# Kernel tuning notes

Measured on AMD Instinct MI355X. Metric: run time of the kernel, lower is better.

Reference implementation:

```python
import jax, jax.numpy as jnp
import numpy as np

D = 256
BN_EPS = 1e-5
EPS = 0.0  # GINEEConv eps buffer, train_eps=False


def setup_inputs() -> dict:
    key = jax.random.key(0)
    ks = jax.random.split(key, 16)
    N, E, G = 60000, 200000, 1500
    node_features = jax.random.normal(ks[0], (N, 92), dtype=jnp.float32)
    edge_index = jax.random.randint(ks[1], (2, E), 0, N)
    atom_weights = jax.random.normal(ks[2], (E, 1), dtype=jnp.float32)
    batch = jnp.sort(jax.random.randint(ks[3], (N,), 0, G))
    s = 0.05
    return {
        "node_features": node_features,
        "edge_index": edge_index,
        "atom_weights": atom_weights,
        "batch": batch,
        "aW": jax.random.normal(ks[4], (92, D), dtype=jnp.float32) * s,
        "ab": jnp.zeros((D,), jnp.float32),
        "eW": jax.random.normal(ks[5], (1, D), dtype=jnp.float32) * s,
        "eb": jnp.zeros((D,), jnp.float32),
        "mlpW": jax.random.normal(ks[6], (3 * D, D), dtype=jnp.float32) * s,
        "mlpb": jnp.zeros((D,), jnp.float32),
        "nnW": jax.random.normal(ks[7], (D, D), dtype=jnp.float32) * s,
        "nnb": jnp.zeros((D,), jnp.float32),
        "bn_g": jax.random.normal(ks[8], (D,), dtype=jnp.float32) * 0.1 + 1.0,
        "bn_b": jax.random.normal(ks[9], (D,), dtype=jnp.float32) * 0.1,
        "bn_m": jax.random.normal(ks[10], (D,), dtype=jnp.float32) * 0.1,
        "bn_v": jax.random.uniform(ks[11], (D,), dtype=jnp.float32) + 0.5,
        "outW": jax.random.normal(ks[12], (D, 6), dtype=jnp.float32) * s,
        "outb": jnp.zeros((6,), jnp.float32),
    }


def _gine_layer(x, e_attr, row, col, mlpW, mlpb, nnW, nnb, bn_g, bn_b, bn_m, bn_v):
    # mlp(cat[x[row], x[col], e_attr]) without materializing the [E,3D] concat
    W1, W2, W3 = mlpW[:D], mlpW[D:2 * D], mlpW[2 * D:]
    new_e = x[row] @ W1 + x[col] @ W2 + e_attr @ W3 + mlpb  # [E, D]
    # message: relu(x_j + edge_attr), x_j = source nodes = edge_index[0]
    msg = jax.nn.relu(x[row] + new_e)  # [E, D]
    agg = jax.ops.segment_sum(msg, col, num_segments=x.shape[0])  # scatter-add to targets
    out = agg + (1.0 + EPS) * x  # residual
    h = out @ nnW + nnb
    h = (h - bn_m) * jax.lax.rsqrt(bn_v + BN_EPS) * bn_g + bn_b  # BN (eval stats)
    return jax.nn.relu(h), new_e


def reference(node_features, edge_index, atom_weights, batch,
              aW, ab, eW, eb, mlpW, mlpb, nnW, nnb,
              bn_g, bn_b, bn_m, bn_v, outW, outb):
    row, col = edge_index[0], edge_index[1]
    x = node_features @ aW + ab            # [N, 256]
    e_attr = atom_weights @ eW + eb        # [E, 256]
    for _ in range(4):  # 4 layers SHARING the same params (ModuleList of same module)
        x, e_attr = _gine_layer(x, e_attr, row, col, mlpW, mlpb, nnW, nnb,
                                bn_g, bn_b, bn_m, bn_v)
    pooled = jax.ops.segment_sum(x, batch, num_segments=1500)  # global_add_pool
    return pooled @ outW + outb  # [G, 6]
```

## Files before the change

### kernel.cpp

```cpp
#include <hip/hip_runtime.h>
#include <stdint.h>

#define DD 256
#define NNODE 60000
#define MPAD 60032
#define NEDGE 200000
#define NGRAPH 1500
#define NCHUNK 59

typedef __bf16 bf16x8 __attribute__((ext_vector_type(8)));
typedef float f32x4 __attribute__((ext_vector_type(4)));
typedef unsigned short us8 __attribute__((ext_vector_type(8)));

__device__ __forceinline__ unsigned short f2bf(float f) {
    union { float f; unsigned int u; } v; v.f = f;
    unsigned int r = v.u + 0x7FFFu + ((v.u >> 16) & 1u);
    return (unsigned short)(r >> 16);
}
__device__ __forceinline__ float bf2f(unsigned short h) {
    union { unsigned int u; float f; } v; v.u = ((unsigned int)h) << 16;
    return v.f;
}
__device__ __forceinline__ void gload_lds16(const void* g, void* l) {
    __builtin_amdgcn_global_load_lds((const __attribute__((address_space(1))) void*)g,
                                     (__attribute__((address_space(3))) void*)l, 16, 0, 0);
}

__global__ __launch_bounds__(256) void prep_weights(const float* __restrict__ mlpW,
                                                    const float* __restrict__ nnW,
                                                    const float* __restrict__ aW,
                                                    const float* __restrict__ ab,
                                                    unsigned short* __restrict__ wc1,
                                                    unsigned short* __restrict__ wc2,
                                                    unsigned short* __restrict__ nnt,
                                                    unsigned short* __restrict__ aWt) {
    int idx = blockIdx.x * 256 + threadIdx.x;
    if (idx < 256 * 512) {
        int n = idx >> 9, k = idx & 511;
        float v1 = (k < 256) ? mlpW[k * DD + n] : mlpW[(k + 256) * DD + n];
        wc1[idx] = f2bf(v1);
        wc2[idx] = f2bf(mlpW[(k + 256) * DD + n]);
    }
    if (idx < 256 * 256) {
        int n = idx >> 8, k = idx & 255;
        nnt[idx] = f2bf(nnW[k * DD + n]);
    }
    if (idx < 256 * 96) {
        int n = idx / 96, k = idx - n * 96;
        float v = (k < 92) ? aW[k * DD + n] : (k == 92 ? ab[n] : 0.0f);
        aWt[idx] = f2bf(v);
    }
}

__global__ __launch_bounds__(256) void prep_uv(const float* __restrict__ eW, const float* __restrict__ eb,
                                               const float* __restrict__ mlpW, const float* __restrict__ mlpb,
                                               const float* __restrict__ nnb,
                                               const float* __restrict__ bn_g, const float* __restrict__ bn_b,
                                               const float* __restrict__ bn_m, const float* __restrict__ bn_v,
                                               float* __restrict__ u_all, float* __restrict__ v_all,
                                               float* __restrict__ scale, float* __restrict__ shift) {
    __shared__ float uc[DD], vc[DD];
    int d = threadIdx.x;
    uc[d] = eW[d];
    vc[d] = eb[d];
    float sc = bn_g[d] * rsqrtf(bn_v[d] + 1e-5f);
    scale[d] = sc;
    shift[d] = (nnb[d] - bn_m[d]) * sc + bn_b[d];
    __syncthreads();
    const float* W3 = mlpW + 2 * DD * DD;
    for (int it = 0; it < 4; ++it) {
        float su = 0.f, sv = 0.f;
        for (int k = 0; k < DD; ++k) {
            float w = W3[k * DD + d];
            su += uc[k] * w;
            sv += vc[k] * w;
        }
        sv += mlpb[d];
        u_all[it * DD + d] = su;
        v_all[it * DD + d] = sv;
        __syncthreads();
        uc[d] = su; vc[d] = sv;
        __syncthreads();
    }
}

__global__ __launch_bounds__(256) void nfb_prep(const float* __restrict__ nf, unsigned short* __restrict__ nfb) {
    int idx = blockIdx.x * 256 + threadIdx.x;
    if (idx >= MPAD * 96) return;
    int r = idx / 96, c = idx - r * 96;
    float v;
    if (r < NNODE && c < 92) v = nf[(size_t)r * 92 + c];
    else v = (c == 92) ? 1.0f : 0.0f;
    nfb[idx] = f2bf(v);
}

__global__ __launch_bounds__(512) void xinit_gemm(const unsigned short* __restrict__ nfb,
                                                  const unsigned short* __restrict__ aWt,
                                                  unsigned short* __restrict__ x) {
    __shared__ unsigned short shmem[(128 + 256) * 96];
    unsigned short (*As)[96] = (unsigned short(*)[96])shmem;
    unsigned short (*Bs)[96] = (unsigned short(*)[96])(shmem + 128 * 96);
    const int tid = threadIdx.x;
    const int lane = tid & 63, wid = tid >> 6;
    const int wr = wid >> 2, wc = wid & 3;
    const int m0 = blockIdx.x * 128;
    const int lr = lane & 15, lq = lane >> 4;

    for (int i = tid; i < 128 * 12; i += 512) {
        int row = i / 12, ch = (i - row * 12) * 8;
        gload_lds16(nfb + (size_t)(m0 + row) * 96 + ch, &As[row][ch]);
    }
    for (int i = tid; i < 256 * 12; i += 512) {
        int row = i / 12, ch = (i - row * 12) * 8;
        gload_lds16(aWt + (size_t)row * 96 + ch, &Bs[row][ch]);
    }
    __syncthreads();

    f32x4 acc[4][4];
    #pragma unroll
    for (int m = 0; m < 4; ++m)
        #pragma unroll
        for (int n = 0; n < 4; ++n) { f32x4 z = {0.f,0.f,0.f,0.f}; acc[m][n] = z; }

    #pragma unroll
    for (int h = 0; h < 3; ++h) {
        bf16x8 af[4], bf[4];
        #pragma unroll
        for (int m = 0; m < 4; ++m)
            af[m] = *reinterpret_cast<const bf16x8*>(&As[wr * 64 + m * 16 + lr][h * 32 + lq * 8]);
        #pragma unroll
        for (int n = 0; n < 4; ++n)
            bf[n] = *reinterpret_cast<const bf16x8*>(&Bs[wc * 64 + n * 16 + lr][h * 32 + lq * 8]);
        #pragma unroll
        for (int m = 0; m < 4; ++m)
            #pragma unroll
            for (int n = 0; n < 4; ++n)
                acc[m][n] = __builtin_amdgcn_mfma_f32_16x16x32_bf16(af[m], bf[n], acc[m][n], 0, 0, 0);
    }
    __syncthreads();

    unsigned short* stg = shmem;
    #pragma unroll
    for (int half = 0; half < 2; ++half) {
        if (wr == half) {
            #pragma unroll
            for (int m = 0; m < 4; ++m)
                #pragma unroll
                for (int n = 0; n < 4; ++n) {
                    const int cs = (wc * 64 + n * 16 + lr) ^ (lq << 4);
                    #pragma unroll
                    for (int j = 0; j < 4; ++j)
                        stg[(m * 16 + lq * 4 + j) * 256 + cs] = f2bf(acc[m][n][j]);
                }
        }
        __syncthreads();
        const int rbase = m0 + half * 64;
        #pragma unroll
        for (int t = 0; t < 4; ++t) {
            int tt = tid + t * 512;
            int rl = tt >> 5, ch = tt & 31;
            int chs = ch ^ (((rl >> 2) & 3) << 1);
            us8 pv = *(const us8*)&stg[rl * 256 + chs * 8];
            ((us8*)x)[(size_t)(rbase + rl) * 32 + ch] = pv;
        }
        __syncthreads();
    }
}

__global__ __launch_bounds__(256) void hist_kernel(const int* __restrict__ ei, int* __restrict__ counts) {
    int e = blockIdx.x * 256 + threadIdx.x;
    if (e < NEDGE) atomicAdd(&counts[ei[NEDGE + e]], 1);
}

__global__ __launch_bounds__(256) void scan1(const int* __restrict__ counts, int* __restrict__ blockSums) {
    int t = threadIdx.x;
    int base = blockIdx.x * 1024 + t * 4;
    int s = 0;
    #pragma unroll
    for (int i = 0; i < 4; ++i) { int idx = base + i; if (idx < NNODE) s += counts[idx]; }
    __shared__ int red[256];
    red[t] = s; __syncthreads();
    for (int d = 128; d; d >>= 1) { if (t < d) red[t] += red[t + d]; __syncthreads(); }
    if (t == 0) blockSums[blockIdx.x] = red[0];
}

__global__ __launch_bounds__(64) void scan2(int* __restrict__ blockSums) {
    int t = threadIdx.x;
    int v = (t < NCHUNK) ? blockSums[t] : 0;
    int orig = v;
    #pragma unroll
    for (int d = 1; d < 64; d <<= 1) {
        int o = __shfl_up(v, d);
        if (t >= d) v += o;
    }
    if (t < NCHUNK) blockSums[t] = v - orig;
}

__global__ __launch_bounds__(256) void scan3(const int* __restrict__ counts, const int* __restrict__ blockSums,
                                             int* __restrict__ offsets, int* __restrict__ cursor) {
    int t = threadIdx.x;
    int base = blockIdx.x * 1024 + t * 4;
    int c[4]; int s = 0;
    #pragma unroll
    for (int i = 0; i < 4; ++i) { int idx = base + i; c[i] = (idx < NNODE) ? counts[idx] : 0; s += c[i]; }
    __shared__ int lds[256];
    lds[t] = s; __syncthreads();
    for (int d = 1; d < 256; d <<= 1) {
        int v = (t >= d) ? lds[t - d] : 0;
        __syncthreads();
        lds[t] += v;
        __syncthreads();
    }
    int off = blockSums[blockIdx.x] + lds[t] - s;
    #pragma unroll
    for (int i = 0; i < 4; ++i) {
        int idx = base + i;
        if (idx < NNODE) { offsets[idx] = off; cursor[idx] = off; off += c[i]; }
    }
}

__global__ __launch_bounds__(256) void scatter_kernel(const int* __restrict__ ei, const float* __restrict__ aw,
                                                      int* __restrict__ cursor,
                                                      int* __restrict__ srow, float* __restrict__ sw) {
    int e = blockIdx.x * 256 + threadIdx.x;
    if (e < NEDGE) {
        int c = ei[NEDGE + e];
        int pos = atomicAdd(&cursor[c], 1);
        srow[pos] = ei[e];
        sw[pos] = aw[e];
    }
}

__global__ __launch_bounds__(512) void gemm_pq(const unsigned short* __restrict__ X,
                                               const unsigned short* __restrict__ Pst,
                                               const unsigned short* __restrict__ Qst,
                                               const unsigned short* __restrict__ B1,
                                               const unsigned short* __restrict__ B2,
                                               unsigned short* __restrict__ Pout,
                                               unsigned short* __restrict__ PXout,
                                               unsigned short* __restrict__ Qout,
                                               const float* __restrict__ cq,
                                               int Ktot) {
    __shared__ unsigned short shmem[(128 + 256) * 64];
    unsigned short (*As)[64] = (unsigned short(*)[64])shmem;
    unsigned short (*Bs)[64] = (unsigned short(*)[64])(shmem + 128 * 64);
    const int b = blockIdx.x;
    const int pairb = b >> 4, jj = b & 15;
    const int sel = jj >> 3, sub = jj & 7;
    const int mb = pairb * 8 + sub;
    if (mb >= MPAD / 128) return;
    const int m0 = mb * 128;

    const unsigned short* A1 = sel ? Qst : Pst;
    const unsigned short* Bt = sel ? B2 : B1;

    const int tid = threadIdx.x;
    const int lane = tid & 63, wid = tid >> 6;
    const int wr = wid >> 2, wc = wid & 3;
    const int lr = lane & 15, lq = lane >> 4;
    const int srow = tid >> 3;
    const int jphys = tid & 7;
    const int jlog = jphys ^ (srow & 7);
    const int scol_g = jlog * 8;
    const int scol_l = jphys * 8;
    const int xorj = (lr & 7);

    f32x4 acc[4][4];
    #pragma unroll
    for (int m = 0; m < 4; ++m)
        #pragma unroll
        for (int n = 0; n < 4; ++n) { f32x4 z = {0.f,0.f,0.f,0.f}; acc[m][n] = z; }

    const int nk = Ktot >> 6;
    for (int kt = 0; kt < nk; ++kt) {
        const int k0 = kt << 6;
        const unsigned short* Ap; int ka;
        if (k0 < 256) { Ap = X; ka = k0; } else { Ap = A1; ka = k0 - 256; }
        #pragma unroll
        for (int p = 0; p < 2; ++p) {
            int row = p * 64 + srow;
            gload_lds16(Ap + (size_t)(m0 + row) * DD + ka + scol_g, &As[row][scol_l]);
        }
        #pragma unroll
        for (int p = 0; p < 4; ++p) {
            int row = p * 64 + srow;
            gload_lds16(Bt + (size_t)row * 512 + k0 + scol_g, &Bs[row][scol_l]);
        }
        __syncthreads();
        #pragma unroll
        for (int h = 0; h < 2; ++h) {
            const int jp = ((h * 4 + lq) ^ xorj) * 8;
            bf16x8 af[4], bfr[4];
            #pragma unroll
            for (int m = 0; m < 4; ++m)
                af[m] = *reinterpret_cast<const bf16x8*>(&As[wr * 64 + m * 16 + lr][jp]);
            #pragma unroll
            for (int n = 0; n < 4; ++n)
                bfr[n] = *reinterpret_cast<const bf16x8*>(&Bs[wc * 64 + n * 16 + lr][jp]);
            #pragma unroll
            for (int m = 0; m < 4; ++m)
                #pragma unroll
                for (int n = 0; n < 4; ++n)
                    acc[m][n] = __builtin_amdgcn_mfma_f32_16x16x32_bf16(af[m], bfr[n], acc[m][n], 0, 0, 0);
        }
        __syncthreads();
    }

    float cqv[4];
    if (sel) {
        #pragma unroll
        for (int n = 0; n < 4; ++n) cqv[n] = cq[wc * 64 + n * 16 + lr];
    }
    unsigned short* stg = shmem;
    #pragma unroll
    for (int half = 0; half < 2; ++half) {
        if (wr == half) {
            #pragma unroll
            for (int m = 0; m < 4; ++m)
                #pragma unroll
                for (int n = 0; n < 4; ++n) {
                    const int cs = (wc * 64 + n * 16 + lr) ^ (lq << 4);
                    #pragma unroll
                    for (int j = 0; j < 4; ++j) {
                        float v = acc[m][n][j];
                        if (sel) v += cqv[n];
                        stg[(m * 16 + lq * 4 + j) * 256 + cs] = f2bf(v);
                    }
                }
        }
        __syncthreads();
        const int rbase = m0 + half * 64;
        #pragma unroll
        for (int t = 0; t < 4; ++t) {
            int tt = tid + t * 512;
            int rl = tt >> 5, ch = tt & 31;
            int chs = ch ^ (((rl >> 2) & 3) << 1);
            us8 pv = *(const us8*)&stg[rl * 256 + chs * 8];
            size_t gidx = (size_t)(rbase + rl) * 32 + ch;
            if (sel == 0) {
                us8 xv = ((const us8*)X)[gidx];
                us8 o;
                #pragma unroll
                for (int c = 0; c < 8; ++c) o[c] = f2bf(bf2f(pv[c]) + bf2f(xv[c]));
                ((us8*)Pout)[gidx] = pv;
                ((us8*)PXout)[gidx] = o;
            } else {
                ((us8*)Qout)[gidx] = pv;
            }
        }
        __syncthreads();
    }
}

__global__ __launch_bounds__(512) void gemm_bn(const unsigned short* __restrict__ A,
                                               const unsigned short* __restrict__ Bt,
                                               unsigned short* __restrict__ Cout,
                                               const float* __restrict__ scale,
                                               const float* __restrict__ shift) {
    __shared__ unsigned short shmem[(128 + 256) * 64];
    unsigned short (*As)[64] = (unsigned short(*)[64])shmem;
    unsigned short (*Bs)[64] = (unsigned short(*)[64])(shmem + 128 * 64);
    const int tid = threadIdx.x;
    const int lane = tid & 63, wid = tid >> 6;
    const int wr = wid >> 2, wc = wid & 3;
    const int m0 = blockIdx.x * 128;
    const int lr = lane & 15, lq = lane >> 4;
    const int srow = tid >> 3;
    const int jphys = tid & 7;
    const int jlog = jphys ^ (srow & 7);
    const int scol_g = jlog * 8;
    const int scol_l = jphys * 8;
    const int xorj = (lr & 7);

    f32x4 acc[4][4];
    #pragma unroll
    for (int m = 0; m < 4; ++m)
        #pragma unroll
        for (int n = 0; n < 4; ++n) { f32x4 z = {0.f,0.f,0.f,0.f}; acc[m][n] = z; }

    for (int kt = 0; kt < 4; ++kt) {
        const int k0 = kt << 6;
        #pragma unroll
        for (int p = 0; p < 2; ++p) {
            int row = p * 64 + srow;
            gload_lds16(A + (size_t)(m0 + row) * DD + k0 + scol_g, &As[row][scol_l]);
        }
        #pragma unroll
        for (int p = 0; p < 4; ++p) {
            int row = p * 64 + srow;
            gload_lds16(Bt + (size_t)row * DD + k0 + scol_g, &Bs[row][scol_l]);
        }
        __syncthreads();
        #pragma unroll
        for (int h = 0; h < 2; ++h) {
            const int jp = ((h * 4 + lq) ^ xorj) * 8;
            bf16x8 af[4], bfr[4];
            #pragma unroll
            for (int m = 0; m < 4; ++m)
                af[m] = *reinterpret_cast<const bf16x8*>(&As[wr * 64 + m * 16 + lr][jp]);
            #pragma unroll
            for (int n = 0; n < 4; ++n)
                bfr[n] = *reinterpret_cast<const bf16x8*>(&Bs[wc * 64 + n * 16 + lr][jp]);
            #pragma unroll
            for (int m = 0; m < 4; ++m)
                #pragma unroll
                for (int n = 0; n < 4; ++n)
                    acc[m][n] = __builtin_amdgcn_mfma_f32_16x16x32_bf16(af[m], bfr[n], acc[m][n], 0, 0, 0);
        }
        __syncthreads();
    }

    float scl[4], shf[4];
    #pragma unroll
    for (int n = 0; n < 4; ++n) {
        int c = wc * 64 + n * 16 + lr;
        scl[n] = scale[c]; shf[n] = shift[c];
    }
    unsigned short* stg = shmem;
    #pragma unroll
    for (int half = 0; half < 2; ++half) {
        if (wr == half) {
            #pragma unroll
            for (int m = 0; m < 4; ++m)
                #pragma unroll
                for (int n = 0; n < 4; ++n) {
                    const int cs = (wc * 64 + n * 16 + lr) ^ (lq << 4);
                    #pragma unroll
                    for (int j = 0; j < 4; ++j) {
                        float y = fmaxf(acc[m][n][j] * scl[n] + shf[n], 0.f);
                        stg[(m * 16 + lq * 4 + j) * 256 + cs] = f2bf(y);
                    }
                }
        }
        __syncthreads();
        const int rbase = m0 + half * 64;
        #pragma unroll
        for (int t = 0; t < 4; ++t) {
            int tt = tid + t * 512;
            int rl = tt >> 5, ch = tt & 31;
            int chs = ch ^ (((rl >> 2) & 3) << 1);
            us8 pv = *(const us8*)&stg[rl * 256 + chs * 8];
            ((us8*)Cout)[(size_t)(rbase + rl) * 32 + ch] = pv;
        }
        __syncthreads();
    }
}

__global__ __launch_bounds__(256) void edge_csr(const int* __restrict__ offsets, const int* __restrict__ counts,
                                                const int* __restrict__ srow, const float* __restrict__ sw,
                                                const unsigned short* __restrict__ X,
                                                const unsigned short* __restrict__ PX,
                                                const unsigned short* __restrict__ Qv,
                                                const float* __restrict__ u,
                                                unsigned short* __restrict__ aggB) {
    const int lane = threadIdx.x & 63, wid = threadIdx.x >> 6;
    const int n = blockIdx.x * 4 + wid;
    if (n >= NNODE) return;
    const int start = offsets[n];
    const int deg = counts[n];
    const int sub = lane & 31, h = lane >> 5;

    const us8* PX8 = (const us8*)PX;

    float4 u0 = ((const float4*)u)[sub * 2], u1 = ((const float4*)u)[sub * 2 + 1];
    float uu[8] = {u0.x, u0.y, u0.z, u0.w, u1.x, u1.y, u1.z, u1.w};

    us8 qv = ((const us8*)Qv)[(size_t)n * 32 + sub];
    float qb[8];
    #pragma unroll
    for (int c = 0; c < 8; ++c) qb[c] = bf2f(qv[c]);

    float a[8];
    us8 xv = ((const us8*)X)[(size_t)n * 32 + sub];
    #pragma unroll
    for (int c = 0; c < 8; ++c) a[c] = (h == 0) ? bf2f(xv[c]) : 0.f;

    for (int b0 = 0; b0 < deg; b0 += 64) {
        int m = deg - b0; if (m > 64) m = 64;
        int myr = 0; float myw = 0.f;
        if (lane < m) { myr = srow[start + b0 + lane]; myw = sw[start + b0 + lane]; }
        int iters = (m + 1) >> 1;
        for (int j = 0; j < iters; ++j) {
            int el = 2 * j + h;
            int r = __shfl(myr, el);
            float w = __shfl(myw, el);
            if (el < m) {
                us8 p2 = PX8[(size_t)r * 32 + sub];
                #pragma unroll
                for (int c = 0; c < 8; ++c)
                    a[c] += fmaxf(bf2f(p2[c]) + qb[c] + w * uu[c], 0.f);
            }
        }
    }
    #pragma unroll
    for (int c = 0; c < 8; ++c) a[c] += __shfl_xor(a[c], 32);
    if (h == 0) {
        us8 o;
        #pragma unroll
        for (int c = 0; c < 8; ++c) o[c] = f2bf(a[c]);
        ((us8*)aggB)[(size_t)n * 32 + sub] = o;
    }
}

__global__ __launch_bounds__(256) void pool_kernel(const unsigned short* __restrict__ x,
                                                   const int* __restrict__ batch,
                                                   float* __restrict__ pooled) {
    const int lane = threadIdx.x & 63, wid = threadIdx.x >> 6;
    const int base = (blockIdx.x * 4 + wid) * 8;
    float4 acc = make_float4(0.f, 0.f, 0.f, 0.f);
    int gcur = -1;
    for (int i = 0; i < 8; ++i) {
        int n = base + i;
        if (n >= NNODE) break;
        int g = batch[n];
        if (g != gcur) {
            if (gcur >= 0) {
                float* pp = pooled + (size_t)gcur * DD + lane * 4;
                unsafeAtomicAdd(pp + 0, acc.x);
                unsafeAtomicAdd(pp + 1, acc.y);
                unsafeAtomicAdd(pp + 2, acc.z);
                unsafeAtomicAdd(pp + 3, acc.w);
            }
            gcur = g;
            acc = make_float4(0.f, 0.f, 0.f, 0.f);
        }
        ushort4 xv = ((const ushort4*)x)[(size_t)n * 64 + lane];
        acc.x += bf2f(xv.x); acc.y += bf2f(xv.y);
        acc.z += bf2f(xv.z); acc.w += bf2f(xv.w);
    }
    if (gcur >= 0) {
        float* pp = pooled + (size_t)gcur * DD + lane * 4;
        unsafeAtomicAdd(pp + 0, acc.x);
        unsafeAtomicAdd(pp + 1, acc.y);
        unsafeAtomicAdd(pp + 2, acc.z);
        unsafeAtomicAdd(pp + 3, acc.w);
    }
}

__global__ __launch_bounds__(64) void out_kernel(const float* __restrict__ pooled,
                                                 const float* __restrict__ outW,
                                                 const float* __restrict__ outb,
                                                 float* __restrict__ out) {
    const int g = blockIdx.x, lane = threadIdx.x;
    float4 p = ((const float4*)pooled)[g * 64 + lane];
    float s[6];
    #pragma unroll
    for (int j = 0; j < 6; ++j) {
        float a = p.x * outW[(lane * 4 + 0) * 6 + j] + p.y * outW[(lane * 4 + 1) * 6 + j] +
                  p.z * outW[(lane * 4 + 2) * 6 + j] + p.w * outW[(lane * 4 + 3) * 6 + j];
        #pragma unroll
        for (int off = 32; off; off >>= 1) a += __shfl_down(a, off);
        s[j] = a;
    }
    if (lane == 0) {
        #pragma unroll
        for (int j = 0; j < 6; ++j) out[g * 6 + j] = s[j] + outb[j];
    }
}

extern "C" void kernel_launch(void* const* d_in, const int* in_sizes, int n_in,
                              void* d_out, int out_size, void* d_ws, size_t ws_size,
                              hipStream_t stream) {
    const float* nf    = (const float*)d_in[0];
    const int*   ei    = (const int*)d_in[1];
    const float* aw    = (const float*)d_in[2];
    const int*   batch = (const int*)d_in[3];
    const float* aW    = (const float*)d_in[4];
    const float* ab    = (const float*)d_in[5];
    const float* eW    = (const float*)d_in[6];
    const float* eb    = (const float*)d_in[7];
    const float* mlpW  = (const float*)d_in[8];
    const float* mlpb  = (const float*)d_in[9];
    const float* nnW   = (const float*)d_in[10];
    const float* nnb   = (const float*)d_in[11];
    const float* bn_g  = (const float*)d_in[12];
    const float* bn_b  = (const float*)d_in[13];
    const float* bn_m  = (const float*)d_in[14];
    const float* bn_v  = (const float*)d_in[15];
    const float* outW  = (const float*)d_in[16];
    const float* outb  = (const float*)d_in[17];
    float* out = (float*)d_out;

    char* ws = (char*)d_ws;
    size_t off = 0;
    auto alloc = [&](size_t bytes) -> void* {
        void* p = ws + off;
        off += (bytes + 255) & ~(size_t)255;
        return p;
    };
    unsigned short* x    = (unsigned short*)alloc((size_t)MPAD * DD * 2);
    unsigned short* P    = (unsigned short*)alloc((size_t)MPAD * DD * 2);
    unsigned short* Qv   = (unsigned short*)alloc((size_t)MPAD * DD * 2);
    unsigned short* aggB = (unsigned short*)alloc((size_t)MPAD * DD * 2);
    unsigned short* PX   = (unsigned short*)alloc((size_t)MPAD * DD * 2);
    unsigned short* nfb  = PX;
    unsigned short* wc1  = (unsigned short*)alloc(256 * 512 * 2);
    unsigned short* wc2  = (unsigned short*)alloc(256 * 512 * 2);
    unsigned short* nnt  = (unsigned short*)alloc(256 * 256 * 2);
    unsigned short* aWt  = (unsigned short*)alloc(256 * 96 * 2);
    float* u_all = (float*)alloc(4 * DD * 4);
    float* v_all = (float*)alloc(4 * DD * 4);
    float* scale = (float*)alloc(DD * 4);
    float* shift = (float*)alloc(DD * 4);
    float* pooled = (float*)alloc((size_t)NGRAPH * DD * 4);
    int* counts  = (int*)alloc((size_t)NNODE * 4);
    int* offsets = (int*)alloc((size_t)NNODE * 4);
    int* cursor  = (int*)alloc((size_t)NNODE * 4);
    int* blockSums = (int*)alloc(NCHUNK * 4);
    int* srowB   = (int*)alloc((size_t)NEDGE * 4);
    float* swB   = (float*)alloc((size_t)NEDGE * 4);
    (void)ws_size; (void)in_sizes; (void)n_in; (void)out_size;

    prep_weights<<<512, 256, 0, stream>>>(mlpW, nnW, aW, ab, wc1, wc2, nnt, aWt);
    prep_uv<<<1, 256, 0, stream>>>(eW, eb, mlpW, mlpb, nnb, bn_g, bn_b, bn_m, bn_v,
                                   u_all, v_all, scale, shift);
    nfb_prep<<<(MPAD * 96 + 255) / 256, 256, 0, stream>>>(nf, nfb);
    xinit_gemm<<<MPAD / 128, 512, 0, stream>>>(nfb, aWt, x);

    hipMemsetAsync(counts, 0, (size_t)NNODE * 4, stream);
    hist_kernel<<<(NEDGE + 255) / 256, 256, 0, stream>>>(ei, counts);
    scan1<<<NCHUNK, 256, 0, stream>>>(counts, blockSums);
    scan2<<<1, 64, 0, stream>>>(blockSums);
    scan3<<<NCHUNK, 256, 0, stream>>>(counts, blockSums, offsets, cursor);
    scatter_kernel<<<(NEDGE + 255) / 256, 256, 0, stream>>>(ei, aw, cursor, srowB, swB);

    const int npairs = (MPAD / 128 + 7) / 8;
    for (int k = 0; k < 4; ++k) {
        gemm_pq<<<npairs * 16, 512, 0, stream>>>(x, P, Qv, wc1, wc2, P, PX, Qv,
                                                 k == 0 ? v_all : mlpb, k ? 512 : 256);
        edge_csr<<<(NNODE + 3) / 4, 256, 0, stream>>>(offsets, counts, srowB, swB, x, PX, Qv,
                                                      u_all + k * DD, aggB);
        gemm_bn<<<MPAD / 128, 512, 0, stream>>>(aggB, nnt, x, scale, shift);
    }

    hipMemsetAsync(pooled, 0, (size_t)NGRAPH * DD * 4, stream);
    pool_kernel<<<(NNODE + 31) / 32, 256, 0, stream>>>(x, batch, pooled);
    out_kernel<<<NGRAPH, 64, 0, stream>>>(pooled, outW, outb, out);
}
```

Before: 511.0 us.

## Fuse CSR edge aggregation with node GEMM and batch-norm epilogue

Merges the per-node edge aggregation kernel and the subsequent node GEMM+BN+ReLU kernel into one kernel. Each 512-thread block gathers 64 nodes' aggregated messages straight into LDS, then multiplies them by the nnW tile and writes the activated result over x in place. This drops the aggB global buffer's write and read and one launch per layer. In exchange, each block uses 64 KB of LDS, which lowers occupancy for the latency-bound gather phase. Each wave also walks 8 nodes serially, so degree imbalance can stall the whole block before the GEMM.

```diff
diff --git a/kernel.cpp b/kernel.cpp
--- a/kernel.cpp
+++ b/kernel.cpp
@@ -352,153 +352,143 @@
     }
 }
 
-__global__ __launch_bounds__(512) void gemm_bn(const unsigned short* __restrict__ A,
+__global__ __launch_bounds__(512) void edge_bn(const int* __restrict__ offsets, const int* __restrict__ counts,
+                                               const int* __restrict__ srow, const float* __restrict__ sw,
+                                               const unsigned short* __restrict__ X,
+                                               const unsigned short* __restrict__ PX,
+                                               const unsigned short* __restrict__ Qv,
+                                               const float* __restrict__ u,
                                                const unsigned short* __restrict__ Bt,
-                                               unsigned short* __restrict__ Cout,
+                                               unsigned short* __restrict__ Xout,
                                                const float* __restrict__ scale,
                                                const float* __restrict__ shift) {
-    __shared__ unsigned short shmem[(128 + 256) * 64];
-    unsigned short (*As)[64] = (unsigned short(*)[64])shmem;
-    unsigned short (*Bs)[64] = (unsigned short(*)[64])(shmem + 128 * 64);
+    __shared__ unsigned short aggL[64 * 256];
+    __shared__ unsigned short Bs[256 * 64];
     const int tid = threadIdx.x;
     const int lane = tid & 63, wid = tid >> 6;
-    const int wr = wid >> 2, wc = wid & 3;
-    const int m0 = blockIdx.x * 128;
+    const int m0 = blockIdx.x * 64;
+    const int sub = lane & 31, h = lane >> 5;
+    const int srowi = tid >> 3;
+    const int jphys = tid & 7;
+    const int jlog = jphys ^ (srowi & 7);
+
+    #pragma unroll
+    for (int p = 0; p < 4; ++p) {
+        int row = p * 64 + srowi;
+        gload_lds16(Bt + (size_t)row * DD + jlog * 8, &Bs[row * 64 + jphys * 8]);
+    }
+
+    float4 u0 = ((const float4*)u)[sub * 2], u1 = ((const float4*)u)[sub * 2 + 1];
+    float uu[8] = {u0.x, u0.y, u0.z, u0.w, u1.x, u1.y, u1.z, u1.w};
+    const us8* PX8 = (const us8*)PX;
+
+    for (int i = 0; i < 8; ++i) {
+        const int rl = wid * 8 + i;
+        const int n = m0 + rl;
+        const int deg = (n < NNODE) ? counts[n] : 0;
+        const int start = (n < NNODE) ? offsets[n] : 0;
+        us8 qv = ((const us8*)Qv)[(size_t)n * 32 + sub];
+        float qb[8];
+        #pragma unroll
+        for (int c = 0; c < 8; ++c) qb[c] = bf2f(qv[c]);
+        us8 xv = ((const us8*)X)[(size_t)n * 32 + sub];
+        float a[8];
+        #pragma unroll
+        for (int c = 0; c < 8; ++c) a[c] = (h == 0) ? bf2f(xv[c]) : 0.f;
+
+        for (int b0 = 0; b0 < deg; b0 += 64) {
+            int m = deg - b0; if (m > 64) m = 64;
+            int myr = 0; float myw = 0.f;
+            if (lane < m) { myr = srow[start + b0 + lane]; myw = sw[start + b0 + lane]; }
+            int iters = (m + 1) >> 1;
+            for (int j = 0; j < iters; ++j) {
+                int el = 2 * j + h;
+                int r = __shfl(myr, el);
+                float w = __shfl(myw, el);
+                if (el < m) {
+                    us8 p2 = PX8[(size_t)r * 32 + sub];
+                    #pragma unroll
+                    for (int c = 0; c < 8; ++c)
+                        a[c] += fmaxf(bf2f(p2[c]) + qb[c] + w * uu[c], 0.f);
+                }
+            }
+        }
+        #pragma unroll
+        for (int c = 0; c < 8; ++c) a[c] += __shfl_xor(a[c], 32);
+        if (h == 0) {
+            us8 o;
+            #pragma unroll
+            for (int c = 0; c < 8; ++c) o[c] = f2bf(a[c]);
+            const int pc = sub ^ (rl & 7);
+            *(us8*)&aggL[rl * 256 + pc * 8] = o;
+        }
+    }
+    __syncthreads();
+
     const int lr = lane & 15, lq = lane >> 4;
-    const int srow = tid >> 3;
-    const int jphys = tid & 7;
-    const int jlog = jphys ^ (srow & 7);
-    const int scol_g = jlog * 8;
-    const int scol_l = jphys * 8;
-    const int xorj = (lr & 7);
-
-    f32x4 acc[4][4];
+    const int xorj = lr & 7;
+    f32x4 acc[4][2];
     #pragma unroll
     for (int m = 0; m < 4; ++m)
         #pragma unroll
-        for (int n = 0; n < 4; ++n) { f32x4 z = {0.f,0.f,0.f,0.f}; acc[m][n] = z; }
+        for (int nf = 0; nf < 2; ++nf) { f32x4 z = {0.f,0.f,0.f,0.f}; acc[m][nf] = z; }
 
     for (int kt = 0; kt < 4; ++kt) {
-        const int k0 = kt << 6;
-        #pragma unroll
-        for (int p = 0; p < 2; ++p) {
-            int row = p * 64 + srow;
-            gload_lds16(A + (size_t)(m0 + row) * DD + k0 + scol_g, &As[row][scol_l]);
-        }
-        #pragma unroll
-        for (int p = 0; p < 4; ++p) {
-            int row = p * 64 + srow;
-            gload_lds16(Bt + (size_t)row * DD + k0 + scol_g, &Bs[row][scol_l]);
-        }
-        __syncthreads();
-        #pragma unroll
-        for (int h = 0; h < 2; ++h) {
-            const int jp = ((h * 4 + lq) ^ xorj) * 8;
-            bf16x8 af[4], bfr[4];
+        if (kt) {
+            __syncthreads();
+            #pragma unroll
+            for (int p = 0; p < 4; ++p) {
+                int row = p * 64 + srowi;
+                gload_lds16(Bt + (size_t)row * DD + kt * 64 + jlog * 8, &Bs[row * 64 + jphys * 8]);
+            }
+            __syncthreads();
+        }
+        #pragma unroll
+        for (int hh = 0; hh < 2; ++hh) {
+            bf16x8 af[4], bfr[2];
             #pragma unroll
             for (int m = 0; m < 4; ++m)
-                af[m] = *reinterpret_cast<const bf16x8*>(&As[wr * 64 + m * 16 + lr][jp]);
-            #pragma unroll
-            for (int n = 0; n < 4; ++n)
-                bfr[n] = *reinterpret_cast<const bf16x8*>(&Bs[wc * 64 + n * 16 + lr][jp]);
+                af[m] = *reinterpret_cast<const bf16x8*>(
+                    &aggL[(m * 16 + lr) * 256 + (((kt * 8 + hh * 4 + lq) ^ xorj) * 8)]);
+            #pragma unroll
+            for (int nf = 0; nf < 2; ++nf)
+                bfr[nf] = *reinterpret_cast<const bf16x8*>(
+                    &Bs[(wid * 32 + nf * 16 + lr) * 64 + (((hh * 4 + lq) ^ xorj) * 8)]);
             #pragma unroll
             for (int m = 0; m < 4; ++m)
                 #pragma unroll
-                for (int n = 0; n < 4; ++n)
-                    acc[m][n] = __builtin_amdgcn_mfma_f32_16x16x32_bf16(af[m], bfr[n], acc[m][n], 0, 0, 0);
-        }
-        __syncthreads();
-    }
-
-    float scl[4], shf[4];
-    #pragma unroll
-    for (int n = 0; n < 4; ++n) {
-        int c = wc * 64 + n * 16 + lr;
-        scl[n] = scale[c]; shf[n] = shift[c];
-    }
-    unsigned short* stg = shmem;
-    #pragma unroll
-    for (int half = 0; half < 2; ++half) {
-        if (wr == half) {
-            #pragma unroll
-            for (int m = 0; m < 4; ++m)
-                #pragma unroll
-                for (int n = 0; n < 4; ++n) {
-                    const int cs = (wc * 64 + n * 16 + lr) ^ (lq << 4);
-                    #pragma unroll
-                    for (int j = 0; j < 4; ++j) {
-                        float y = fmaxf(acc[m][n][j] * scl[n] + shf[n], 0.f);
-                        stg[(m * 16 + lq * 4 + j) * 256 + cs] = f2bf(y);
-                    }
-                }
-        }
-        __syncthreads();
-        const int rbase = m0 + half * 64;
-        #pragma unroll
-        for (int t = 0; t < 4; ++t) {
-            int tt = tid + t * 512;
-            int rl = tt >> 5, ch = tt & 31;
-            int chs = ch ^ (((rl >> 2) & 3) << 1);
-            us8 pv = *(const us8*)&stg[rl * 256 + chs * 8];
-            ((us8*)Cout)[(size_t)(rbase + rl) * 32 + ch] = pv;
-        }
-        __syncthreads();
-    }
-}
-
-__global__ __launch_bounds__(256) void edge_csr(const int* __restrict__ offsets, const int* __restrict__ counts,
-                                                const int* __restrict__ srow, const float* __restrict__ sw,
-                                                const unsigned short* __restrict__ X,
-                                                const unsigned short* __restrict__ PX,
-                                                const unsigned short* __restrict__ Qv,
-                                                const float* __restrict__ u,
-                                                unsigned short* __restrict__ aggB) {
-    const int lane = threadIdx.x & 63, wid = threadIdx.x >> 6;
-    const int n = blockIdx.x * 4 + wid;
-    if (n >= NNODE) return;
-    const int start = offsets[n];
-    const int deg = counts[n];
-    const int sub = lane & 31, h = lane >> 5;
-
-    const us8* PX8 = (const us8*)PX;
-
-    float4 u0 = ((const float4*)u)[sub * 2], u1 = ((const float4*)u)[sub * 2 + 1];
-    float uu[8] = {u0.x, u0.y, u0.z, u0.w, u1.x, u1.y, u1.z, u1.w};
-
-    us8 qv = ((const us8*)Qv)[(size_t)n * 32 + sub];
-    float qb[8];
-    #pragma unroll
-    for (int c = 0; c < 8; ++c) qb[c] = bf2f(qv[c]);
-
-    float a[8];
-    us8 xv = ((const us8*)X)[(size_t)n * 32 + sub];
-    #pragma unroll
-    for (int c = 0; c < 8; ++c) a[c] = (h == 0) ? bf2f(xv[c]) : 0.f;
-
-    for (int b0 = 0; b0 < deg; b0 += 64) {
-        int m = deg - b0; if (m > 64) m = 64;
-        int myr = 0; float myw = 0.f;
-        if (lane < m) { myr = srow[start + b0 + lane]; myw = sw[start + b0 + lane]; }
-        int iters = (m + 1) >> 1;
-        for (int j = 0; j < iters; ++j) {
-            int el = 2 * j + h;
-            int r = __shfl(myr, el);
-            float w = __shfl(myw, el);
-            if (el < m) {
-                us8 p2 = PX8[(size_t)r * 32 + sub];
-                #pragma unroll
-                for (int c = 0; c < 8; ++c)
-                    a[c] += fmaxf(bf2f(p2[c]) + qb[c] + w * uu[c], 0.f);
+                for (int nf = 0; nf < 2; ++nf)
+                    acc[m][nf] = __builtin_amdgcn_mfma_f32_16x16x32_bf16(af[m], bfr[nf], acc[m][nf], 0, 0, 0);
+        }
+    }
+    __syncthreads();
+
+    float scl[2], shf[2];
+    #pragma unroll
+    for (int nf = 0; nf < 2; ++nf) {
+        int c = wid * 32 + nf * 16 + lr;
+        scl[nf] = scale[c]; shf[nf] = shift[c];
+    }
+    unsigned short* stg = Bs;
+    #pragma unroll
+    for (int m = 0; m < 4; ++m)
+        #pragma unroll
+        for (int nf = 0; nf < 2; ++nf) {
+            const int cs = (wid * 32 + nf * 16 + lr) ^ (lq << 4);
+            #pragma unroll
+            for (int j = 0; j < 4; ++j) {
+                float y = fmaxf(acc[m][nf][j] * scl[nf] + shf[nf], 0.f);
+                stg[(m * 16 + lq * 4 + j) * 256 + cs] = f2bf(y);
             }
         }
-    }
-    #pragma unroll
-    for (int c = 0; c < 8; ++c) a[c] += __shfl_xor(a[c], 32);
-    if (h == 0) {
-        us8 o;
-        #pragma unroll
-        for (int c = 0; c < 8; ++c) o[c] = f2bf(a[c]);
-        ((us8*)aggB)[(size_t)n * 32 + sub] = o;
+    __syncthreads();
+    #pragma unroll
+    for (int t = 0; t < 4; ++t) {
+        int tt = tid + t * 512;
+        int rl = tt >> 5, ch = tt & 31;
+        int chs = ch ^ (((rl >> 2) & 3) << 1);
+        us8 pv = *(const us8*)&stg[rl * 256 + chs * 8];
+        ((us8*)Xout)[(size_t)(m0 + rl) * 32 + ch] = pv;
     }
 }
 
@@ -591,7 +581,6 @@
     unsigned short* x    = (unsigned short*)alloc((size_t)MPAD * DD * 2);
     unsigned short* P    = (unsigned short*)alloc((size_t)MPAD * DD * 2);
     unsigned short* Qv   = (unsigned short*)alloc((size_t)MPAD * DD * 2);
-    unsigned short* aggB = (unsigned short*)alloc((size_t)MPAD * DD * 2);
     unsigned short* PX   = (unsigned short*)alloc((size_t)MPAD * DD * 2);
     unsigned short* nfb  = PX;
     unsigned short* wc1  = (unsigned short*)alloc(256 * 512 * 2);
@@ -628,9 +617,8 @@
     for (int k = 0; k < 4; ++k) {
         gemm_pq<<<npairs * 16, 512, 0, stream>>>(x, P, Qv, wc1, wc2, P, PX, Qv,
                                                  k == 0 ? v_all : mlpb, k ? 512 : 256);
-        edge_csr<<<(NNODE + 3) / 4, 256, 0, stream>>>(offsets, counts, srowB, swB, x, PX, Qv,
-                                                      u_all + k * DD, aggB);
-        gemm_bn<<<MPAD / 128, 512, 0, stream>>>(aggB, nnt, x, scale, shift);
+        edge_bn<<<MPAD / 64, 512, 0, stream>>>(offsets, counts, srowB, swB, x, PX, Qv,
+                                               u_all + k * DD, nnt, x, scale, shift);
     }
 
     hipMemsetAsync(pooled, 0, (size_t)NGRAPH * DD * 4, stream);
```

After: 518.6 us. No clear change (+1.5%).

## Double-buffer LDS tiles with K=32 steps in gemm_pq and gemm_bn

Applied to the files above, without the earlier changes.

Both MFMA GEMM kernels now stage K-slices of 32 into two ping-pong LDS buffers. The global-to-LDS loads for the next slice are issued before the MFMAs on the current one, followed by a single waitcnt and barrier per step. The goal is to hide global load latency behind compute instead of stalling on a sync after each load. In exchange there are twice as many iterations and barriers, and the XOR swizzle for 32-wide rows changes, which could bring back LDS bank conflicts.

```diff
diff --git a/kernel.cpp b/kernel.cpp
--- a/kernel.cpp
+++ b/kernel.cpp
@@ -241,9 +241,7 @@
                                                unsigned short* __restrict__ Qout,
                                                const float* __restrict__ cq,
                                                int Ktot) {
-    __shared__ unsigned short shmem[(128 + 256) * 64];
-    unsigned short (*As)[64] = (unsigned short(*)[64])shmem;
-    unsigned short (*Bs)[64] = (unsigned short(*)[64])(shmem + 128 * 64);
+    __shared__ unsigned short shmem[2 * 384 * 32];
     const int b = blockIdx.x;
     const int pairb = b >> 4, jj = b & 15;
     const int sel = jj >> 3, sub = jj & 7;
@@ -258,52 +256,59 @@
     const int lane = tid & 63, wid = tid >> 6;
     const int wr = wid >> 2, wc = wid & 3;
     const int lr = lane & 15, lq = lane >> 4;
-    const int srow = tid >> 3;
-    const int jphys = tid & 7;
-    const int jlog = jphys ^ (srow & 7);
-    const int scol_g = jlog * 8;
-    const int scol_l = jphys * 8;
-    const int xorj = (lr & 7);
-
-    f32x4 acc[4][4];
-    #pragma unroll
-    for (int m = 0; m < 4; ++m)
-        #pragma unroll
-        for (int n = 0; n < 4; ++n) { f32x4 z = {0.f,0.f,0.f,0.f}; acc[m][n] = z; }
-
-    const int nk = Ktot >> 6;
-    for (int kt = 0; kt < nk; ++kt) {
-        const int k0 = kt << 6;
+    const int srowA = tid >> 2;
+    const int jphys = tid & 3;
+    const int jlogA = jphys ^ ((srowA >> 1) & 3);
+
+    auto stage = [&](int kt, int buf) {
+        const int k0 = kt << 5;
         const unsigned short* Ap; int ka;
         if (k0 < 256) { Ap = X; ka = k0; } else { Ap = A1; ka = k0 - 256; }
+        unsigned short* base = shmem + buf * 12288;
+        gload_lds16(Ap + (size_t)(m0 + srowA) * DD + ka + jlogA * 8, base + srowA * 32 + jphys * 8);
         #pragma unroll
         for (int p = 0; p < 2; ++p) {
-            int row = p * 64 + srow;
-            gload_lds16(Ap + (size_t)(m0 + row) * DD + ka + scol_g, &As[row][scol_l]);
-        }
-        #pragma unroll
-        for (int p = 0; p < 4; ++p) {
-            int row = p * 64 + srow;
-            gload_lds16(Bt + (size_t)row * 512 + k0 + scol_g, &Bs[row][scol_l]);
-        }
-        __syncthreads();
-        #pragma unroll
-        for (int h = 0; h < 2; ++h) {
-            const int jp = ((h * 4 + lq) ^ xorj) * 8;
-            bf16x8 af[4], bfr[4];
-            #pragma unroll
-            for (int m = 0; m < 4; ++m)
-                af[m] = *reinterpret_cast<const bf16x8*>(&As[wr * 64 + m * 16 + lr][jp]);
+            int row = p * 128 + srowA;
+            gload_lds16(Bt + (size_t)row * 512 + k0 + jlogA * 8, base + 4096 + row * 32 + jphys * 8);
+        }
+    };
+
+    f32x4 acc[4][4];
+    #pragma unroll
+    for (int m = 0; m < 4; ++m)
+        #pragma unroll
+        for (int n = 0; n < 4; ++n) { f32x4 z = {0.f,0.f,0.f,0.f}; acc[m][n] = z; }
+
+    const int nk = Ktot >> 5;
+    stage(0, 0);
+    asm volatile("s_waitcnt vmcnt(0)" ::: "memory");
+    __builtin_amdgcn_sched_barrier(0);
+    __builtin_amdgcn_s_barrier();
+
+    for (int kt = 0; kt < nk; ++kt) {
+        const int cur = kt & 1;
+        if (kt + 1 < nk) stage(kt + 1, cur ^ 1);
+        __builtin_amdgcn_sched_barrier(0);
+        const unsigned short* base = shmem + cur * 12288;
+        bf16x8 af[4], bfr[4];
+        #pragma unroll
+        for (int m = 0; m < 4; ++m) {
+            int r = wr * 64 + m * 16 + lr;
+            af[m] = *reinterpret_cast<const bf16x8*>(base + r * 32 + ((lq ^ ((r >> 1) & 3)) << 3));
+        }
+        #pragma unroll
+        for (int n = 0; n < 4; ++n) {
+            int r = wc * 64 + n * 16 + lr;
+            bfr[n] = *reinterpret_cast<const bf16x8*>(base + 4096 + r * 32 + ((lq ^ ((r >> 1) & 3)) << 3));
+        }
+        #pragma unroll
+        for (int m = 0; m < 4; ++m)
             #pragma unroll
             for (int n = 0; n < 4; ++n)
-                bfr[n] = *reinterpret_cast<const bf16x8*>(&Bs[wc * 64 + n * 16 + lr][jp]);
-            #pragma unroll
-            for (int m = 0; m < 4; ++m)
-                #pragma unroll
-                for (int n = 0; n < 4; ++n)
-                    acc[m][n] = __builtin_amdgcn_mfma_f32_16x16x32_bf16(af[m], bfr[n], acc[m][n], 0, 0, 0);
-        }
-        __syncthreads();
+                acc[m][n] = __builtin_amdgcn_mfma_f32_16x16x32_bf16(af[m], bfr[n], acc[m][n], 0, 0, 0);
+        asm volatile("s_waitcnt vmcnt(0)" ::: "memory");
+        __builtin_amdgcn_sched_barrier(0);
+        __builtin_amdgcn_s_barrier();
     }
 
     float cqv[4];
@@ -357,20 +362,26 @@
                                                unsigned short* __restrict__ Cout,
                                                const float* __restrict__ scale,
                                                const float* __restrict__ shift) {
-    __shared__ unsigned short shmem[(128 + 256) * 64];
-    unsigned short (*As)[64] = (unsigned short(*)[64])shmem;
-    unsigned short (*Bs)[64] = (unsigned short(*)[64])(shmem + 128 * 64);
+    __shared__ unsigned short shmem[2 * 384 * 32];
     const int tid = threadIdx.x;
     const int lane = tid & 63, wid = tid >> 6;
     const int wr = wid >> 2, wc = wid & 3;
     const int m0 = blockIdx.x * 128;
     const int lr = lane & 15, lq = lane >> 4;
-    const int srow = tid >> 3;
-    const int jphys = tid & 7;
-    const int jlog = jphys ^ (srow & 7);
-    const int scol_g = jlog * 8;
-    const int scol_l = jphys * 8;
-    const int xorj = (lr & 7);
+    const int srowA = tid >> 2;
+    const int jphys = tid & 3;
+    const int jlogA = jphys ^ ((srowA >> 1) & 3);
+
+    auto stage = [&](int kt, int buf) {
+        const int k0 = kt << 5;
+        unsigned short* base = shmem + buf * 12288;
+        gload_lds16(A + (size_t)(m0 + srowA) * DD + k0 + jlogA * 8, base + srowA * 32 + jphys * 8);
+        #pragma unroll
+        for (int p = 0; p < 2; ++p) {
+            int row = p * 128 + srowA;
+            gload_lds16(Bt + (size_t)row * DD + k0 + jlogA * 8, base + 4096 + row * 32 + jphys * 8);
+        }
+    };
 
     f32x4 acc[4][4];
     #pragma unroll
@@ -378,36 +389,36 @@
         #pragma unroll
         for (int n = 0; n < 4; ++n) { f32x4 z = {0.f,0.f,0.f,0.f}; acc[m][n] = z; }
 
-    for (int kt = 0; kt < 4; ++kt) {
-        const int k0 = kt << 6;
-        #pragma unroll
-        for (int p = 0; p < 2; ++p) {
-            int row = p * 64 + srow;
-            gload_lds16(A + (size_t)(m0 + row) * DD + k0 + scol_g, &As[row][scol_l]);
-        }
-        #pragma unroll
-        for (int p = 0; p < 4; ++p) {
-            int row = p * 64 + srow;
-            gload_lds16(Bt + (size_t)row * DD + k0 + scol_g, &Bs[row][scol_l]);
-        }
-        __syncthreads();
-        #pragma unroll
-        for (int h = 0; h < 2; ++h) {
-            const int jp = ((h * 4 + lq) ^ xorj) * 8;
-            bf16x8 af[4], bfr[4];
-            #pragma unroll
-            for (int m = 0; m < 4; ++m)
-                af[m] = *reinterpret_cast<const bf16x8*>(&As[wr * 64 + m * 16 + lr][jp]);
+    const int nk = 8;
+    stage(0, 0);
+    asm volatile("s_waitcnt vmcnt(0)" ::: "memory");
+    __builtin_amdgcn_sched_barrier(0);
+    __builtin_amdgcn_s_barrier();
+
+    for (int kt = 0; kt < nk; ++kt) {
+        const int cur = kt & 1;
+        if (kt + 1 < nk) stage(kt + 1, cur ^ 1);
+        __builtin_amdgcn_sched_barrier(0);
+        const unsigned short* base = shmem + cur * 12288;
+        bf16x8 af[4], bfr[4];
+        #pragma unroll
+        for (int m = 0; m < 4; ++m) {
+            int r = wr * 64 + m * 16 + lr;
+            af[m] = *reinterpret_cast<const bf16x8*>(base + r * 32 + ((lq ^ ((r >> 1) & 3)) << 3));
+        }
+        #pragma unroll
+        for (int n = 0; n < 4; ++n) {
+            int r = wc * 64 + n * 16 + lr;
+            bfr[n] = *reinterpret_cast<const bf16x8*>(base + 4096 + r * 32 + ((lq ^ ((r >> 1) & 3)) << 3));
+        }
+        #pragma unroll
+        for (int m = 0; m < 4; ++m)
             #pragma unroll
             for (int n = 0; n < 4; ++n)
-                bfr[n] = *reinterpret_cast<const bf16x8*>(&Bs[wc * 64 + n * 16 + lr][jp]);
-            #pragma unroll
-            for (int m = 0; m < 4; ++m)
-                #pragma unroll
-                for (int n = 0; n < 4; ++n)
-                    acc[m][n] = __builtin_amdgcn_mfma_f32_16x16x32_bf16(af[m], bfr[n], acc[m][n], 0, 0, 0);
-        }
-        __syncthreads();
+                acc[m][n] = __builtin_amdgcn_mfma_f32_16x16x32_bf16(af[m], bfr[n], acc[m][n], 0, 0, 0);
+        asm volatile("s_waitcnt vmcnt(0)" ::: "memory");
+        __builtin_amdgcn_sched_barrier(0);
+        __builtin_amdgcn_s_barrier();
     }
 
     float scl[4], shf[4];
```

After: 588.4 us. 15.1% more time.
